# Kernel optimization log

Measured on AMD Instinct MI355X. Metric: run time of the kernel, lower is better.

## Reference

```python
import jax, jax.numpy as jnp
import numpy as np


def _identity_grid(B, D, H, W):
    # F.affine_grid(eye, [B, 3, D, H, W], align_corners=True):
    # grid[..., 0]=x over W, grid[..., 1]=y over H, grid[..., 2]=z over D, all in [-1, 1]
    zs = jnp.linspace(-1.0, 1.0, D, dtype=jnp.float32)
    ys = jnp.linspace(-1.0, 1.0, H, dtype=jnp.float32)
    xs = jnp.linspace(-1.0, 1.0, W, dtype=jnp.float32)
    gz, gy, gx = jnp.meshgrid(zs, ys, xs, indexing='ij')
    grid = jnp.stack([gx, gy, gz], axis=-1)  # [D, H, W, 3]
    return jnp.broadcast_to(grid[None], (B, D, H, W, 3))


def grid_sample_3d(vol, coords):
    """Bilinear (trilinear) grid_sample, align_corners=True, zeros padding.
    vol:    [B, D, H, W, C] channels-last volume
    coords: [B, D, H, W, 3] normalized (x, y, z) in [-1, 1]
    """
    B, D, H, W, C = vol.shape
    x = (coords[..., 0] + 1.0) * 0.5 * (W - 1)
    y = (coords[..., 1] + 1.0) * 0.5 * (H - 1)
    z = (coords[..., 2] + 1.0) * 0.5 * (D - 1)
    x0 = jnp.floor(x); x1 = x0 + 1.0
    y0 = jnp.floor(y); y1 = y0 + 1.0
    z0 = jnp.floor(z); z1 = z0 + 1.0
    wx = x - x0; wy = y - y0; wz = z - z0

    def gather(zi, yi, xi):
        valid = ((xi >= 0) & (xi <= W - 1) & (yi >= 0) & (yi <= H - 1)
                 & (zi >= 0) & (zi <= D - 1)).astype(vol.dtype)
        xc = jnp.clip(xi, 0, W - 1).astype(jnp.int32)
        yc = jnp.clip(yi, 0, H - 1).astype(jnp.int32)
        zc = jnp.clip(zi, 0, D - 1).astype(jnp.int32)
        vals = jax.vmap(lambda v, z_, y_, x_: v[z_, y_, x_])(vol, zc, yc, xc)  # [B,D,H,W,C]
        return vals * valid[..., None]

    out = (gather(z0, y0, x0) * ((1 - wz) * (1 - wy) * (1 - wx))[..., None]
         + gather(z0, y0, x1) * ((1 - wz) * (1 - wy) * wx)[..., None]
         + gather(z0, y1, x0) * ((1 - wz) * wy * (1 - wx))[..., None]
         + gather(z0, y1, x1) * ((1 - wz) * wy * wx)[..., None]
         + gather(z1, y0, x0) * (wz * (1 - wy) * (1 - wx))[..., None]
         + gather(z1, y0, x1) * (wz * (1 - wy) * wx)[..., None]
         + gather(z1, y1, x0) * (wz * wy * (1 - wx))[..., None]
         + gather(z1, y1, x1) * (wz * wy * wx)[..., None])
    return out


def setup_inputs() -> dict:
    key = jax.random.key(0)
    B, D, H, W = 1, 160, 160, 160
    velocity_field = 0.05 * jax.random.normal(key, (B, D, H, W, 3), dtype=jnp.float32)
    grid = _identity_grid(B, D, H, W)
    return {"velocity_field": velocity_field, "grid": grid, "n": 6}


def reference(velocity_field, grid, n):
    """Scaling-and-squaring exponential map (GeodesicShooting.get_warp).
    Returns the integrated displacement field [B, D, H, W, 3]."""
    v = velocity_field * (1.0 / (2 ** n))
    for _ in range(n):
        v = v + grid_sample_3d(v, grid + v)
    return v
```

## Files before the change

### kernel.cpp

```cpp
#include <hip/hip_runtime.h>

#define DD 160
#define HH 160
#define WW 160
#define NVOX (DD * HH * WW)
#define NBLOCK (NVOX / 256)
#define HALF_EXTENT 79.5f

template <bool SCALE_SRC, bool NT_OUT>
__global__ __launch_bounds__(256) void gs_step(const float* __restrict__ vin,
                                               float* __restrict__ vout,
                                               float s) {
    int bid = blockIdx.x;
    int swz = (bid & 7) * (NBLOCK >> 3) + (bid >> 3);
    int tid = swz * 256 + (int)threadIdx.x;

    int x = tid % WW;
    int t = tid / WW;
    int y = t % HH;
    int z = t / HH;

    int base = tid * 3;
    float vx = vin[base + 0];
    float vy = vin[base + 1];
    float vz = vin[base + 2];
    if (SCALE_SRC) { vx *= s; vy *= s; vz *= s; }

    float fx = fmaf(vx, HALF_EXTENT, (float)x);
    float fy = fmaf(vy, HALF_EXTENT, (float)y);
    float fz = fmaf(vz, HALF_EXTENT, (float)z);

    float x0f = floorf(fx), y0f = floorf(fy), z0f = floorf(fz);
    float wx = fx - x0f, wy = fy - y0f, wz = fz - z0f;
    int x0 = (int)x0f, y0 = (int)y0f, z0 = (int)z0f;
    int x1 = x0 + 1, y1 = y0 + 1, z1 = z0 + 1;

    float ax0 = (x0 >= 0 && x0 < WW) ? (1.0f - wx) : 0.0f;
    float ax1 = (x1 >= 0 && x1 < WW) ? wx : 0.0f;
    float ay0 = (y0 >= 0 && y0 < HH) ? (1.0f - wy) : 0.0f;
    float ay1 = (y1 >= 0 && y1 < HH) ? wy : 0.0f;
    float az0 = (z0 >= 0 && z0 < DD) ? (1.0f - wz) : 0.0f;
    float az1 = (z1 >= 0 && z1 < DD) ? wz : 0.0f;

    int x0c = min(max(x0, 0), WW - 1), x1c = min(max(x1, 0), WW - 1);
    int y0c = min(max(y0, 0), HH - 1), y1c = min(max(y1, 0), HH - 1);
    int z0c = min(max(z0, 0), DD - 1), z1c = min(max(z1, 0), DD - 1);

    int zs0 = z0c * (HH * WW), zs1 = z1c * (HH * WW);
    int ys0 = y0c * WW,        ys1 = y1c * WW;

    const float* p000 = vin + (size_t)(zs0 + ys0 + x0c) * 3;
    const float* p001 = vin + (size_t)(zs0 + ys0 + x1c) * 3;
    const float* p010 = vin + (size_t)(zs0 + ys1 + x0c) * 3;
    const float* p011 = vin + (size_t)(zs0 + ys1 + x1c) * 3;
    const float* p100 = vin + (size_t)(zs1 + ys0 + x0c) * 3;
    const float* p101 = vin + (size_t)(zs1 + ys0 + x1c) * 3;
    const float* p110 = vin + (size_t)(zs1 + ys1 + x0c) * 3;
    const float* p111 = vin + (size_t)(zs1 + ys1 + x1c) * 3;

    float a0 = p000[0], a1 = p000[1], a2 = p000[2];
    float b0 = p001[0], b1 = p001[1], b2 = p001[2];
    float c0 = p010[0], c1 = p010[1], c2 = p010[2];
    float d0 = p011[0], d1 = p011[1], d2 = p011[2];
    float e0 = p100[0], e1 = p100[1], e2 = p100[2];
    float f0 = p101[0], f1 = p101[1], f2 = p101[2];
    float g0 = p110[0], g1 = p110[1], g2 = p110[2];
    float h0 = p111[0], h1 = p111[1], h2 = p111[2];

    float w000 = az0 * ay0 * ax0;
    float w001 = az0 * ay0 * ax1;
    float w010 = az0 * ay1 * ax0;
    float w011 = az0 * ay1 * ax1;
    float w100 = az1 * ay0 * ax0;
    float w101 = az1 * ay0 * ax1;
    float w110 = az1 * ay1 * ax0;
    float w111 = az1 * ay1 * ax1;

    float acc0 = w000 * a0;
    float acc1 = w000 * a1;
    float acc2 = w000 * a2;
    acc0 = fmaf(w001, b0, acc0); acc1 = fmaf(w001, b1, acc1); acc2 = fmaf(w001, b2, acc2);
    acc0 = fmaf(w010, c0, acc0); acc1 = fmaf(w010, c1, acc1); acc2 = fmaf(w010, c2, acc2);
    acc0 = fmaf(w011, d0, acc0); acc1 = fmaf(w011, d1, acc1); acc2 = fmaf(w011, d2, acc2);
    acc0 = fmaf(w100, e0, acc0); acc1 = fmaf(w100, e1, acc1); acc2 = fmaf(w100, e2, acc2);
    acc0 = fmaf(w101, f0, acc0); acc1 = fmaf(w101, f1, acc1); acc2 = fmaf(w101, f2, acc2);
    acc0 = fmaf(w110, g0, acc0); acc1 = fmaf(w110, g1, acc1); acc2 = fmaf(w110, g2, acc2);
    acc0 = fmaf(w111, h0, acc0); acc1 = fmaf(w111, h1, acc1); acc2 = fmaf(w111, h2, acc2);

    if (SCALE_SRC) { acc0 *= s; acc1 *= s; acc2 *= s; }

    float r0 = vx + acc0, r1 = vy + acc1, r2 = vz + acc2;

    if (NT_OUT) {
        __builtin_nontemporal_store(r0, &vout[base + 0]);
        __builtin_nontemporal_store(r1, &vout[base + 1]);
        __builtin_nontemporal_store(r2, &vout[base + 2]);
    } else {
        vout[base + 0] = r0;
        vout[base + 1] = r1;
        vout[base + 2] = r2;
    }
}

__global__ __launch_bounds__(256) void gs_init_scale(const float* __restrict__ in,
                                                     float* __restrict__ out,
                                                     int n4, float s) {
    int i = blockIdx.x * blockDim.x + threadIdx.x;
    if (i < n4) {
        float4 v = reinterpret_cast<const float4*>(in)[i];
        v.x *= s; v.y *= s; v.z *= s; v.w *= s;
        reinterpret_cast<float4*>(out)[i] = v;
    }
}

extern "C" void kernel_launch(void* const* d_in, const int* in_sizes, int n_in,
                              void* d_out, int out_size, void* d_ws, size_t ws_size,
                              hipStream_t stream) {
    const float* vel = (const float*)d_in[0];
    float* out = (float*)d_out;

    const float scale = 1.0f / 64.0f;
    dim3 blk(256);
    dim3 grd(NBLOCK);

    const size_t buf_bytes = (size_t)NVOX * 3 * sizeof(float);

    if (ws_size >= 2 * buf_bytes) {
        float* A = (float*)d_ws;
        float* B = (float*)((char*)d_ws + buf_bytes);

        gs_step<true,  false><<<grd, blk, 0, stream>>>(vel, A, scale);
        gs_step<false, false><<<grd, blk, 0, stream>>>(A, B, scale);
        gs_step<false, false><<<grd, blk, 0, stream>>>(B, A, scale);
        gs_step<false, false><<<grd, blk, 0, stream>>>(A, B, scale);
        gs_step<false, false><<<grd, blk, 0, stream>>>(B, A, scale);
        gs_step<false, true><<<grd, blk, 0, stream>>>(A, out, scale);
    } else {
        float* ws = (float*)d_ws;
        const int n4 = NVOX * 3 / 4;
        dim3 grd_init((n4 + 255) / 256);

        gs_init_scale<<<grd_init, blk, 0, stream>>>(vel, out, n4, scale);

        float* src = out;
        float* dst = ws;
        for (int i = 0; i < 6; ++i) {
            gs_step<false, false><<<grd, blk, 0, stream>>>(src, dst, scale);
            float* tmp = src; src = dst; dst = tmp;
        }
    }
}
```

Before: 340.5 us.

## Stage 3D halo tiles in LDS for trilinear gathers with global fallback

Adds a tiled kernel in which each block loads an 8x8x16 voxel tile plus a halo into shared memory, then serves the eight trilinear corner reads from LDS when the sample point falls inside the staged box. Points outside the box fall back to global gathers. The goal is to replace scattered, poorly coalesced global loads with one coalesced tile load per block. The cost is redundant halo loading (13x13x21 versus 8x8x16 voxels), an added barrier, LDS bank conflicts from the stride-3 layout, and lower occupancy from about 40KB of LDS per block. The final step still uses the old gather kernel with non-temporal stores.

Result: slower. 407.7 us (+19.7%).

```diff
diff --git a/kernel.cpp b/kernel.cpp
--- a/kernel.cpp
+++ b/kernel.cpp
@@ -7,10 +7,158 @@
 #define NBLOCK (NVOX / 256)
 #define HALF_EXTENT 79.5f
 
+#define TZ 8
+#define TY 8
+#define TX 16
+#define NTZ (DD / TZ)
+#define NTY (HH / TY)
+#define NTX (WW / TX)
+#define NBLK_T (NTZ * NTY * NTX)
+#define SZC (TZ + 5)
+#define SYC (TY + 5)
+#define SXC (TX + 5)
+#define NSROW (SZC * SYC)
+#define LDSF (SZC * SYC * SXC * 3)
+#define XSTR 3
+#define YSTR (SXC * 3)
+#define ZSTR (SYC * SXC * 3)
+
+template <bool SCALE_SRC>
+__global__ __launch_bounds__(256) void gs_step_lds(const float* __restrict__ vin,
+                                                   float* __restrict__ vout,
+                                                   float s) {
+    int bid = blockIdx.x;
+    int swz = (bid & 7) * (NBLK_T >> 3) + (bid >> 3);
+    int tx = swz % NTX;
+    int tyz = swz / NTX;
+    int ty = tyz % NTY;
+    int tz = tyz / NTY;
+
+    int zlo = tz * TZ - 2, ylo = ty * TY - 2, xlo = tx * TX - 2;
+
+    __shared__ float ls[LDSF];
+
+    int t = threadIdx.x;
+    int wave = t >> 6, lane = t & 63;
+
+    int rowSub = lane / 21;
+    int xi = lane - rowSub * 21;
+    if (rowSub < 3) {
+#pragma unroll 5
+        for (int j = 0; j < 15; ++j) {
+            int tri = wave + j * 4;
+            int r = tri * 3 + rowSub;
+            if (r < NSROW) {
+                int sz = r / SYC, sy = r - sz * SYC;
+                int gz = min(max(zlo + sz, 0), DD - 1);
+                int gy = min(max(ylo + sy, 0), HH - 1);
+                int gx = min(max(xlo + xi, 0), WW - 1);
+                const float* p = vin + (size_t)((gz * HH + gy) * WW + gx) * 3;
+                float v0 = p[0], v1 = p[1], v2 = p[2];
+                int d = (r * SXC + xi) * 3;
+                ls[d + 0] = v0; ls[d + 1] = v1; ls[d + 2] = v2;
+            }
+        }
+    }
+    __syncthreads();
+
+#pragma unroll
+    for (int k = 0; k < 4; ++k) {
+        int l = k * 256 + t;
+        int lx = l & (TX - 1);
+        int ly = (l >> 4) & (TY - 1);
+        int lz = l >> 7;
+        int x = tx * TX + lx, y = ty * TY + ly, z = tz * TZ + lz;
+
+        size_t base = (size_t)((z * HH + y) * WW + x) * 3;
+        float vx = vin[base + 0];
+        float vy = vin[base + 1];
+        float vz = vin[base + 2];
+        if (SCALE_SRC) { vx *= s; vy *= s; vz *= s; }
+
+        float fx = fmaf(vx, HALF_EXTENT, (float)x);
+        float fy = fmaf(vy, HALF_EXTENT, (float)y);
+        float fz = fmaf(vz, HALF_EXTENT, (float)z);
+
+        float x0f = floorf(fx), y0f = floorf(fy), z0f = floorf(fz);
+        float wx = fx - x0f, wy = fy - y0f, wz = fz - z0f;
+        int x0 = (int)x0f, y0 = (int)y0f, z0 = (int)z0f;
+        int x1 = x0 + 1, y1 = y0 + 1, z1 = z0 + 1;
+
+        float ax0 = (x0 >= 0 && x0 < WW) ? (1.0f - wx) : 0.0f;
+        float ax1 = (x1 >= 0 && x1 < WW) ? wx : 0.0f;
+        float ay0 = (y0 >= 0 && y0 < HH) ? (1.0f - wy) : 0.0f;
+        float ay1 = (y1 >= 0 && y1 < HH) ? wy : 0.0f;
+        float az0 = (z0 >= 0 && z0 < DD) ? (1.0f - wz) : 0.0f;
+        float az1 = (z1 >= 0 && z1 < DD) ? wz : 0.0f;
+
+        float w000 = az0 * ay0 * ax0, w001 = az0 * ay0 * ax1;
+        float w010 = az0 * ay1 * ax0, w011 = az0 * ay1 * ax1;
+        float w100 = az1 * ay0 * ax0, w101 = az1 * ay0 * ax1;
+        float w110 = az1 * ay1 * ax0, w111 = az1 * ay1 * ax1;
+
+        int zr = z0 - zlo, yr = y0 - ylo, xr = x0 - xlo;
+        bool inbox = ((unsigned)zr <= (unsigned)(SZC - 2)) &
+                     ((unsigned)yr <= (unsigned)(SYC - 2)) &
+                     ((unsigned)xr <= (unsigned)(SXC - 2));
+
+        float acc0, acc1, acc2;
+        if (inbox) {
+            int f = zr * ZSTR + yr * YSTR + xr * XSTR;
+            const float* q000 = ls + f;
+            const float* q001 = q000 + XSTR;
+            const float* q010 = q000 + YSTR;
+            const float* q011 = q000 + YSTR + XSTR;
+            const float* q100 = q000 + ZSTR;
+            const float* q101 = q000 + ZSTR + XSTR;
+            const float* q110 = q000 + ZSTR + YSTR;
+            const float* q111 = q000 + ZSTR + YSTR + XSTR;
+
+            acc0 = w000 * q000[0]; acc1 = w000 * q000[1]; acc2 = w000 * q000[2];
+            acc0 = fmaf(w001, q001[0], acc0); acc1 = fmaf(w001, q001[1], acc1); acc2 = fmaf(w001, q001[2], acc2);
+            acc0 = fmaf(w010, q010[0], acc0); acc1 = fmaf(w010, q010[1], acc1); acc2 = fmaf(w010, q010[2], acc2);
+            acc0 = fmaf(w011, q011[0], acc0); acc1 = fmaf(w011, q011[1], acc1); acc2 = fmaf(w011, q011[2], acc2);
+            acc0 = fmaf(w100, q100[0], acc0); acc1 = fmaf(w100, q100[1], acc1); acc2 = fmaf(w100, q100[2], acc2);
+            acc0 = fmaf(w101, q101[0], acc0); acc1 = fmaf(w101, q101[1], acc1); acc2 = fmaf(w101, q101[2], acc2);
+            acc0 = fmaf(w110, q110[0], acc0); acc1 = fmaf(w110, q110[1], acc1); acc2 = fmaf(w110, q110[2], acc2);
+            acc0 = fmaf(w111, q111[0], acc0); acc1 = fmaf(w111, q111[1], acc1); acc2 = fmaf(w111, q111[2], acc2);
+        } else {
+            int x0c = min(max(x0, 0), WW - 1), x1c = min(max(x1, 0), WW - 1);
+            int y0c = min(max(y0, 0), HH - 1), y1c = min(max(y1, 0), HH - 1);
+            int z0c = min(max(z0, 0), DD - 1), z1c = min(max(z1, 0), DD - 1);
+            int zs0 = z0c * (HH * WW), zs1 = z1c * (HH * WW);
+            int ys0 = y0c * WW,        ys1 = y1c * WW;
+            const float* p000 = vin + (size_t)(zs0 + ys0 + x0c) * 3;
+            const float* p001 = vin + (size_t)(zs0 + ys0 + x1c) * 3;
+            const float* p010 = vin + (size_t)(zs0 + ys1 + x0c) * 3;
+            const float* p011 = vin + (size_t)(zs0 + ys1 + x1c) * 3;
+            const float* p100 = vin + (size_t)(zs1 + ys0 + x0c) * 3;
+            const float* p101 = vin + (size_t)(zs1 + ys0 + x1c) * 3;
+            const float* p110 = vin + (size_t)(zs1 + ys1 + x0c) * 3;
+            const float* p111 = vin + (size_t)(zs1 + ys1 + x1c) * 3;
+
+            acc0 = w000 * p000[0]; acc1 = w000 * p000[1]; acc2 = w000 * p000[2];
+            acc0 = fmaf(w001, p001[0], acc0); acc1 = fmaf(w001, p001[1], acc1); acc2 = fmaf(w001, p001[2], acc2);
+            acc0 = fmaf(w010, p010[0], acc0); acc1 = fmaf(w010, p010[1], acc1); acc2 = fmaf(w010, p010[2], acc2);
+            acc0 = fmaf(w011, p011[0], acc0); acc1 = fmaf(w011, p011[1], acc1); acc2 = fmaf(w011, p011[2], acc2);
+            acc0 = fmaf(w100, p100[0], acc0); acc1 = fmaf(w100, p100[1], acc1); acc2 = fmaf(w100, p100[2], acc2);
+            acc0 = fmaf(w101, p101[0], acc0); acc1 = fmaf(w101, p101[1], acc1); acc2 = fmaf(w101, p101[2], acc2);
+            acc0 = fmaf(w110, p110[0], acc0); acc1 = fmaf(w110, p110[1], acc1); acc2 = fmaf(w110, p110[2], acc2);
+            acc0 = fmaf(w111, p111[0], acc0); acc1 = fmaf(w111, p111[1], acc1); acc2 = fmaf(w111, p111[2], acc2);
+        }
+
+        if (SCALE_SRC) { acc0 *= s; acc1 *= s; acc2 *= s; }
+
+        vout[base + 0] = vx + acc0;
+        vout[base + 1] = vy + acc1;
+        vout[base + 2] = vz + acc2;
+    }
+}
+
 template <bool SCALE_SRC, bool NT_OUT>
-__global__ __launch_bounds__(256) void gs_step(const float* __restrict__ vin,
-                                               float* __restrict__ vout,
-                                               float s) {
+__global__ __launch_bounds__(256) void gs_step_g(const float* __restrict__ vin,
+                                                 float* __restrict__ vout,
+                                                 float s) {
     int bid = blockIdx.x;
     int swz = (bid & 7) * (NBLOCK >> 3) + (bid >> 3);
     int tid = swz * 256 + (int)threadIdx.x;
@@ -67,18 +215,12 @@
     float g0 = p110[0], g1 = p110[1], g2 = p110[2];
     float h0 = p111[0], h1 = p111[1], h2 = p111[2];
 
-    float w000 = az0 * ay0 * ax0;
-    float w001 = az0 * ay0 * ax1;
-    float w010 = az0 * ay1 * ax0;
-    float w011 = az0 * ay1 * ax1;
-    float w100 = az1 * ay0 * ax0;
-    float w101 = az1 * ay0 * ax1;
-    float w110 = az1 * ay1 * ax0;
-    float w111 = az1 * ay1 * ax1;
-
-    float acc0 = w000 * a0;
-    float acc1 = w000 * a1;
-    float acc2 = w000 * a2;
+    float w000 = az0 * ay0 * ax0, w001 = az0 * ay0 * ax1;
+    float w010 = az0 * ay1 * ax0, w011 = az0 * ay1 * ax1;
+    float w100 = az1 * ay0 * ax0, w101 = az1 * ay0 * ax1;
+    float w110 = az1 * ay1 * ax0, w111 = az1 * ay1 * ax1;
+
+    float acc0 = w000 * a0, acc1 = w000 * a1, acc2 = w000 * a2;
     acc0 = fmaf(w001, b0, acc0); acc1 = fmaf(w001, b1, acc1); acc2 = fmaf(w001, b2, acc2);
     acc0 = fmaf(w010, c0, acc0); acc1 = fmaf(w010, c1, acc1); acc2 = fmaf(w010, c2, acc2);
     acc0 = fmaf(w011, d0, acc0); acc1 = fmaf(w011, d1, acc1); acc2 = fmaf(w011, d2, acc2);
@@ -121,7 +263,8 @@
 
     const float scale = 1.0f / 64.0f;
     dim3 blk(256);
-    dim3 grd(NBLOCK);
+    dim3 grd_t(NBLK_T);
+    dim3 grd_g(NBLOCK);
 
     const size_t buf_bytes = (size_t)NVOX * 3 * sizeof(float);
 
@@ -129,12 +272,12 @@
         float* A = (float*)d_ws;
         float* B = (float*)((char*)d_ws + buf_bytes);
 
-        gs_step<true,  false><<<grd, blk, 0, stream>>>(vel, A, scale);
-        gs_step<false, false><<<grd, blk, 0, stream>>>(A, B, scale);
-        gs_step<false, false><<<grd, blk, 0, stream>>>(B, A, scale);
-        gs_step<false, false><<<grd, blk, 0, stream>>>(A, B, scale);
-        gs_step<false, false><<<grd, blk, 0, stream>>>(B, A, scale);
-        gs_step<false, true><<<grd, blk, 0, stream>>>(A, out, scale);
+        gs_step_lds<true ><<<grd_t, blk, 0, stream>>>(vel, A, scale);
+        gs_step_lds<false><<<grd_t, blk, 0, stream>>>(A, B, scale);
+        gs_step_lds<false><<<grd_t, blk, 0, stream>>>(B, A, scale);
+        gs_step_lds<false><<<grd_t, blk, 0, stream>>>(A, B, scale);
+        gs_step_lds<false><<<grd_t, blk, 0, stream>>>(B, A, scale);
+        gs_step_g<false, true><<<grd_g, blk, 0, stream>>>(A, out, scale);
     } else {
         float* ws = (float*)d_ws;
         const int n4 = NVOX * 3 / 4;
@@ -145,7 +288,7 @@
         float* src = out;
         float* dst = ws;
         for (int i = 0; i < 6; ++i) {
-            gs_step<false, false><<<grd, blk, 0, stream>>>(src, dst, scale);
+            gs_step_g<false, false><<<grd_g, blk, 0, stream>>>(src, dst, scale);
             float* tmp = src; src = dst; dst = tmp;
         }
     }
```
